# Kernel tuning notes

Measured on AMD Instinct MI355X. Metric: run time of the kernel, lower is better.

Reference implementation:

```python
import jax, jax.numpy as jnp
import numpy as np

H = 16          # num_heads
D = 4           # att_size (hard-coded in module)
HID = 256       # hidden_size
B, N = 4, 1024
SCALE = D ** (-0.5)
BN_EPS = 1e-5
NEG_SLOPE = 0.2


def setup_inputs() -> dict:
    key = jax.random.key(0)
    ks = jax.random.split(key, 12)
    s = 0.05
    return {
        "q": jax.random.normal(ks[0], (B, HID, N), jnp.float32),
        "k": jax.random.normal(ks[1], (B, HID, N), jnp.float32),
        "v": jax.random.normal(ks[2], (B, HID, N), jnp.float32),
        "attn_bias": jax.random.normal(ks[3], (B, H, N, N), jnp.float32),
        # 1x1 Conv1d weights (kernel dim squeezed): [out_ch, in_ch]
        "Wq": jax.random.normal(ks[4], (H * D, HID), jnp.float32) * s,
        "Wk": jax.random.normal(ks[5], (H * D, HID), jnp.float32) * s,
        "Wv": jax.random.normal(ks[6], (H * D, HID), jnp.float32) * s,
        "Wo": jax.random.normal(ks[7], (HID, H * D), jnp.float32) * s,
        "bo": jax.random.normal(ks[8], (HID,), jnp.float32) * s,
        "gamma": jnp.ones((HID,), jnp.float32),
        "beta": jnp.zeros((HID,), jnp.float32),
        "run_mean": jnp.zeros((HID,), jnp.float32),
        "run_var": jnp.ones((HID,), jnp.float32),
    }


def reference(q, k, v, attn_bias, Wq, Wk, Wv, Wo, bo, gamma, beta, run_mean, run_var):
    # 1x1 conv projections: [B, HID, N] -> [B, H*D, N]
    qp = jnp.einsum('oc,bcn->bon', Wq, q)
    kp = jnp.einsum('oc,bcn->bon', Wk, k)
    vp = jnp.einsum('oc,bcn->bon', Wv, v)
    # faithful (non-standard) view: [B, H*D, N] -> [B, D, N, H]
    qh = qp.reshape(B, D, N, H).transpose(0, 3, 2, 1)   # [B, H, N, D]
    vh = vp.reshape(B, D, N, H).transpose(0, 3, 2, 1)   # [B, H, N, D]
    kh = kp.reshape(B, D, N, H).transpose(0, 3, 1, 2)   # [B, H, D, N]
    # scaled dot-product attention with additive bias
    scores = jnp.einsum('bhnd,bhdm->bhnm', qh, kh) * SCALE + attn_bias
    attn = jax.nn.softmax(scores, axis=-1)              # dropout rate 0.0 (eval)
    x = jnp.einsum('bhnm,bhmd->bhnd', attn, vh)         # [B, H, N, D]
    # transpose(3,2) then view(B, H*D, N)
    x = x.transpose(0, 1, 3, 2).reshape(B, H * D, N)
    # output 1x1 conv + BatchNorm1d (eval, running stats) + LeakyReLU(0.2)
    y = jnp.einsum('oc,bcn->bon', Wo, x) + bo[None, :, None]
    inv = jax.lax.rsqrt(run_var + BN_EPS)
    y = (y - run_mean[None, :, None]) * (gamma * inv)[None, :, None] + beta[None, :, None]
    return jnp.where(y > 0, y, NEG_SLOPE * y)
```

## Files before the change

### kernel.cpp

```cpp
#include <hip/hip_runtime.h>

#define HID 256
#define NSEQ 1024
#define NH 16
#define DH 4
#define NB 4
#define SCALEF 0.5f
#define HEADSZ (NB * NH * NSEQ * DH)

typedef float f4 __attribute__((ext_vector_type(4)));

__global__ __launch_bounds__(256) void proj_kernel(
    const float* __restrict__ q, const float* __restrict__ k,
    const float* __restrict__ v, const float* __restrict__ Wq,
    const float* __restrict__ Wk, const float* __restrict__ Wv,
    float* __restrict__ ws)
{
    const int tid   = threadIdx.x;
    const int pos_l = tid & 63;
    int cb = __builtin_amdgcn_readfirstlane(tid >> 6);
    const int p    = blockIdx.y;
    const int b    = blockIdx.z;
    const int pos0 = blockIdx.x * 64;

    const float* in = (p == 0) ? q : (p == 1) ? k : v;
    const float* W  = (p == 0) ? Wq : (p == 1) ? Wk : Wv;
    float* dst = ws + (size_t)p * HEADSZ;

    __shared__ float lds_in[64][64];

    const int row_l = tid >> 4;
    const int col4  = tid & 15;
    const float* inb = in + (size_t)b * HID * NSEQ + pos0;

    float acc[16];
#pragma unroll
    for (int j = 0; j < 16; ++j) acc[j] = 0.f;

    f4 vbuf[4];
#pragma unroll
    for (int t = 0; t < 4; ++t)
        vbuf[t] = *(const f4*)(inb + (size_t)(row_l + 16 * t) * NSEQ + col4 * 4);

    for (int c = 0; c < 4; ++c) {
#pragma unroll
        for (int t = 0; t < 4; ++t)
            *(f4*)&lds_in[row_l + 16 * t][col4 * 4] = vbuf[t];
        __syncthreads();
        if (c < 3) {
#pragma unroll
            for (int t = 0; t < 4; ++t)
                vbuf[t] = *(const f4*)(inb +
                    (size_t)((c + 1) * 64 + row_l + 16 * t) * NSEQ + col4 * 4);
        }
#pragma unroll
        for (int i8 = 0; i8 < 64; i8 += 8) {
            float x[8];
#pragma unroll
            for (int j = 0; j < 8; ++j) x[j] = lds_in[i8 + j][pos_l];
#pragma unroll
            for (int kk = 0; kk < 16; ++kk) {
                const float* wr = W + (cb * 16 + kk) * HID + c * 64 + i8;
#pragma unroll
                for (int j = 0; j < 8; ++j)
                    acc[kk] = fmaf(wr[j], x[j], acc[kk]);
            }
        }
        __syncthreads();
    }

    const int pos_g = pos0 + pos_l;
    const int h     = pos_g & 15;
    const int nsub  = pos_g >> 4;
#pragma unroll
    for (int kk = 0; kk < 16; ++kk) {
        int c = cb * 16 + kk;
        int d = c >> 4;
        int n = (c & 15) * 64 + nsub;
        dst[(((size_t)b * NH + h) * NSEQ + n) * DH + d] = acc[kk];
    }
}

__global__ __launch_bounds__(256, 3) void attn_kernel(
    const float* __restrict__ bias, const float* __restrict__ ws,
    float* __restrict__ x2)
{
    const int tid  = threadIdx.x;
    const int lane = tid & 63;
    const int wave = tid >> 6;
    const int qg   = lane >> 4;
    const int kg   = lane & 15;
    const int h    = blockIdx.y;
    const int b    = blockIdx.z;
    const int n0   = blockIdx.x * 64 + wave * 16;

    const float4* Qh = (const float4*)(ws);
    const float4* Kh = (const float4*)(ws + (size_t)1 * HEADSZ);
    const float4* Vh = (const float4*)(ws + (size_t)2 * HEADSZ);
    const int headbase = (b * NH + h) * NSEQ;

    float4 q4[4];
#pragma unroll
    for (int r = 0; r < 4; ++r) q4[r] = Qh[headbase + n0 + qg * 4 + r];

    float sum[4];
    float o[4][4];
#pragma unroll
    for (int r = 0; r < 4; ++r) {
        sum[r] = 0.f;
#pragma unroll
        for (int d = 0; d < 4; ++d) o[r][d] = 0.f;
    }

    const float* bbase =
        bias + ((size_t)headbase + n0 + qg * 4) * NSEQ + kg * 4;
    const int kvbase = headbase + kg * 4;

#define LOG2E 1.44269504f
#define EOFF  (-16.f * LOG2E)

    f4 bb[4], bbn[4];
#pragma unroll
    for (int r = 0; r < 4; ++r)
        bb[r] = __builtin_nontemporal_load((const f4*)(bbase + (size_t)r * NSEQ));

    for (int m0 = 0; m0 < NSEQ; m0 += 64) {
        if (m0 + 64 < NSEQ) {
#pragma unroll
            for (int r = 0; r < 4; ++r)
                bbn[r] = __builtin_nontemporal_load(
                    (const f4*)(bbase + (size_t)r * NSEQ + m0 + 64));
        }
        float4 kb[4], vb[4];
#pragma unroll
        for (int i = 0; i < 4; ++i) {
            kb[i] = Kh[kvbase + m0 + i];
            vb[i] = Vh[kvbase + m0 + i];
        }
#pragma unroll
        for (int r = 0; r < 4; ++r) {
            const float be[4] = {bb[r].x, bb[r].y, bb[r].z, bb[r].w};
#pragma unroll
            for (int i = 0; i < 4; ++i) {
                float dot = q4[r].x * kb[i].x + q4[r].y * kb[i].y +
                            q4[r].z * kb[i].z + q4[r].w * kb[i].w;
                float s = fmaf(dot, SCALEF, be[i]);
                float e = exp2f(fmaf(s, LOG2E, EOFF));
                sum[r] += e;
                o[r][0] = fmaf(e, vb[i].x, o[r][0]);
                o[r][1] = fmaf(e, vb[i].y, o[r][1]);
                o[r][2] = fmaf(e, vb[i].z, o[r][2]);
                o[r][3] = fmaf(e, vb[i].w, o[r][3]);
            }
        }
#pragma unroll
        for (int r = 0; r < 4; ++r) bb[r] = bbn[r];
    }

#pragma unroll
    for (int st = 1; st <= 8; st <<= 1) {
#pragma unroll
        for (int r = 0; r < 4; ++r) {
            sum[r]  += __shfl_xor(sum[r],  st, 64);
            o[r][0] += __shfl_xor(o[r][0], st, 64);
            o[r][1] += __shfl_xor(o[r][1], st, 64);
            o[r][2] += __shfl_xor(o[r][2], st, 64);
            o[r][3] += __shfl_xor(o[r][3], st, 64);
        }
    }

    if (kg < 4) {
        float4 wv;
        wv.x = o[0][kg] / sum[0];
        wv.y = o[1][kg] / sum[1];
        wv.z = o[2][kg] / sum[2];
        wv.w = o[3][kg] / sum[3];
        *(float4*)(x2 + ((size_t)b * (NH * DH) + h * DH + kg) * NSEQ
                      + n0 + qg * 4) = wv;
    }
}

__global__ __launch_bounds__(256) void out_kernel(
    const float* __restrict__ x2, const float* __restrict__ Wo,
    const float* __restrict__ bo, const float* __restrict__ gamma,
    const float* __restrict__ beta, const float* __restrict__ rmean,
    const float* __restrict__ rvar, float* __restrict__ out)
{
    const int pos4 = threadIdx.x * 4;
    const int o0   = blockIdx.y * 4;
    const int b    = blockIdx.z;

    const float* xb = x2 + (size_t)b * (NH * DH) * NSEQ;

    f4 acc[4];
#pragma unroll
    for (int j = 0; j < 4; ++j) acc[j] = (f4)(0.f);

#pragma unroll 8
    for (int c = 0; c < NH * DH; ++c) {
        f4 x = *(const f4*)(xb + (size_t)c * NSEQ + pos4);
#pragma unroll
        for (int j = 0; j < 4; ++j)
            acc[j] += Wo[(o0 + j) * (NH * DH) + c] * x;
    }
#pragma unroll
    for (int j = 0; j < 4; ++j) {
        int oc = o0 + j;
        float scale = gamma[oc] * rsqrtf(rvar[oc] + 1e-5f);
        f4 y = (acc[j] + (bo[oc] - rmean[oc])) * scale + beta[oc];
        float* dst = out + ((size_t)b * HID + oc) * NSEQ + pos4;
        f4 res;
#pragma unroll
        for (int d = 0; d < 4; ++d) {
            float yy = y[d];
            res[d] = (yy > 0.f) ? yy : 0.2f * yy;
        }
        *(f4*)dst = res;
    }
}

extern "C" void kernel_launch(void* const* d_in, const int* in_sizes, int n_in,
                              void* d_out, int out_size, void* d_ws, size_t ws_size,
                              hipStream_t stream) {
    const float* q     = (const float*)d_in[0];
    const float* k     = (const float*)d_in[1];
    const float* v     = (const float*)d_in[2];
    const float* bias  = (const float*)d_in[3];
    const float* Wq    = (const float*)d_in[4];
    const float* Wk    = (const float*)d_in[5];
    const float* Wv    = (const float*)d_in[6];
    const float* Wo    = (const float*)d_in[7];
    const float* bo    = (const float*)d_in[8];
    const float* gamma = (const float*)d_in[9];
    const float* beta  = (const float*)d_in[10];
    const float* rmean = (const float*)d_in[11];
    const float* rvar  = (const float*)d_in[12];

    float* ws = (float*)d_ws;
    float* x2 = ws + (size_t)3 * HEADSZ;
    float* out = (float*)d_out;

    proj_kernel<<<dim3(NSEQ / 64, 3, NB), 256, 0, stream>>>(q, k, v, Wq, Wk, Wv, ws);
    attn_kernel<<<dim3(NSEQ / 64, NH, NB), 256, 0, stream>>>(bias, ws, x2);
    out_kernel<<<dim3(1, HID / 4, NB), 256, 0, stream>>>(
        x2, Wo, bo, gamma, beta, rmean, rvar, out);
}
```

Baseline: 135.1 us.

## Remap attention kernel so each wave reads whole bias rows contiguously

Each wave now handles 8 query rows, one at a time. Its 64 lanes cover the full 1024-key row, so each bias load is a fully contiguous 1KB segment instead of 16-lane strips across 4 rows. The grid doubles to 32 queries per block and occupancy is raised to 4 blocks. In exchange, the explicit software prefetch of the next bias tile is dropped, K/V are reloaded for every query row, and the cross-lane reduction grows to 6 shuffle stages over 8 rows. The output is written with scalar stores.

```diff
diff --git a/kernel.cpp b/kernel.cpp
--- a/kernel.cpp
+++ b/kernel.cpp
@@ -81,70 +81,52 @@
     }
 }
 
-__global__ __launch_bounds__(256, 3) void attn_kernel(
+__global__ __launch_bounds__(256, 4) void attn_kernel(
     const float* __restrict__ bias, const float* __restrict__ ws,
     float* __restrict__ x2)
 {
     const int tid  = threadIdx.x;
     const int lane = tid & 63;
     const int wave = tid >> 6;
-    const int qg   = lane >> 4;
-    const int kg   = lane & 15;
     const int h    = blockIdx.y;
     const int b    = blockIdx.z;
-    const int n0   = blockIdx.x * 64 + wave * 16;
+    const int n0   = blockIdx.x * 32 + wave * 8;
 
     const float4* Qh = (const float4*)(ws);
     const float4* Kh = (const float4*)(ws + (size_t)1 * HEADSZ);
     const float4* Vh = (const float4*)(ws + (size_t)2 * HEADSZ);
     const int headbase = (b * NH + h) * NSEQ;
-
-    float4 q4[4];
-#pragma unroll
-    for (int r = 0; r < 4; ++r) q4[r] = Qh[headbase + n0 + qg * 4 + r];
-
-    float sum[4];
-    float o[4][4];
-#pragma unroll
-    for (int r = 0; r < 4; ++r) {
-        sum[r] = 0.f;
-#pragma unroll
-        for (int d = 0; d < 4; ++d) o[r][d] = 0.f;
-    }
-
-    const float* bbase =
-        bias + ((size_t)headbase + n0 + qg * 4) * NSEQ + kg * 4;
-    const int kvbase = headbase + kg * 4;
+    const int mb = lane * 4;
 
 #define LOG2E 1.44269504f
 #define EOFF  (-16.f * LOG2E)
 
-    f4 bb[4], bbn[4];
-#pragma unroll
-    for (int r = 0; r < 4; ++r)
-        bb[r] = __builtin_nontemporal_load((const f4*)(bbase + (size_t)r * NSEQ));
-
-    for (int m0 = 0; m0 < NSEQ; m0 += 64) {
-        if (m0 + 64 < NSEQ) {
-#pragma unroll
-            for (int r = 0; r < 4; ++r)
-                bbn[r] = __builtin_nontemporal_load(
-                    (const f4*)(bbase + (size_t)r * NSEQ + m0 + 64));
-        }
-        float4 kb[4], vb[4];
-#pragma unroll
-        for (int i = 0; i < 4; ++i) {
-            kb[i] = Kh[kvbase + m0 + i];
-            vb[i] = Vh[kvbase + m0 + i];
-        }
-#pragma unroll
-        for (int r = 0; r < 4; ++r) {
-            const float be[4] = {bb[r].x, bb[r].y, bb[r].z, bb[r].w};
+    float sum[8];
+    float o[8][4];
+#pragma unroll
+    for (int r = 0; r < 8; ++r) {
+        sum[r] = 0.f;
+        o[r][0] = o[r][1] = o[r][2] = o[r][3] = 0.f;
+    }
+
+    for (int r = 0; r < 8; ++r) {
+        const int n = n0 + r;
+        const float4 q4 = Qh[headbase + n];
+        const float* brow = bias + ((size_t)headbase + n) * NSEQ + mb;
+#pragma unroll
+        for (int j = 0; j < 4; ++j) {
+            f4 bb = __builtin_nontemporal_load((const f4*)(brow + j * 256));
+            float4 kb[4], vb[4];
 #pragma unroll
             for (int i = 0; i < 4; ++i) {
-                float dot = q4[r].x * kb[i].x + q4[r].y * kb[i].y +
-                            q4[r].z * kb[i].z + q4[r].w * kb[i].w;
-                float s = fmaf(dot, SCALEF, be[i]);
+                kb[i] = Kh[headbase + j * 256 + mb + i];
+                vb[i] = Vh[headbase + j * 256 + mb + i];
+            }
+#pragma unroll
+            for (int i = 0; i < 4; ++i) {
+                float dot = q4.x * kb[i].x + q4.y * kb[i].y +
+                            q4.z * kb[i].z + q4.w * kb[i].w;
+                float s = fmaf(dot, SCALEF, bb[i]);
                 float e = exp2f(fmaf(s, LOG2E, EOFF));
                 sum[r] += e;
                 o[r][0] = fmaf(e, vb[i].x, o[r][0]);
@@ -153,14 +135,12 @@
                 o[r][3] = fmaf(e, vb[i].w, o[r][3]);
             }
         }
-#pragma unroll
-        for (int r = 0; r < 4; ++r) bb[r] = bbn[r];
-    }
-
-#pragma unroll
-    for (int st = 1; st <= 8; st <<= 1) {
-#pragma unroll
-        for (int r = 0; r < 4; ++r) {
+    }
+
+#pragma unroll
+    for (int st = 1; st < 64; st <<= 1) {
+#pragma unroll
+        for (int r = 0; r < 8; ++r) {
             sum[r]  += __shfl_xor(sum[r],  st, 64);
             o[r][0] += __shfl_xor(o[r][0], st, 64);
             o[r][1] += __shfl_xor(o[r][1], st, 64);
@@ -169,14 +149,11 @@
         }
     }
 
-    if (kg < 4) {
-        float4 wv;
-        wv.x = o[0][kg] / sum[0];
-        wv.y = o[1][kg] / sum[1];
-        wv.z = o[2][kg] / sum[2];
-        wv.w = o[3][kg] / sum[3];
-        *(float4*)(x2 + ((size_t)b * (NH * DH) + h * DH + kg) * NSEQ
-                      + n0 + qg * 4) = wv;
+    if (lane < 32) {
+        const int d = lane >> 3;
+        const int r = lane & 7;
+        x2[((size_t)b * (NH * DH) + h * DH + d) * NSEQ + n0 + r] =
+            o[r][d] / sum[r];
     }
 }
 
@@ -241,7 +218,7 @@
     float* out = (float*)d_out;
 
     proj_kernel<<<dim3(NSEQ / 64, 3, NB), 256, 0, stream>>>(q, k, v, Wq, Wk, Wv, ws);
-    attn_kernel<<<dim3(NSEQ / 64, NH, NB), 256, 0, stream>>>(bias, ws, x2);
+    attn_kernel<<<dim3(NSEQ / 32, NH, NB), 256, 0, stream>>>(bias, ws, x2);
     out_kernel<<<dim3(1, HID / 4, NB), 256, 0, stream>>>(
         x2, Wo, bo, gamma, beta, rmean, rvar, out);
 }
```

Measured after the change: 471.4 us. 249% more time.
